# Kernel tuning notes

Hardware: AMD Instinct MI355X
Metric: run time of the kernel (lower is better)

## Reference

```python
import jax, jax.numpy as jnp
import numpy as np

N_NODES = 10000
IN_CH = 512
HID = 128
HEADS = 4
OUT_CH = 256
N_EDGES = 160000
NEG_SLOPE = 0.2  # PyG GATConv default


def gat_conv(x, src, dst, W, a_src, a_dst, b):
    """PyG-style GATConv. x:[N,F_in], W:[F_in,H*C], a_src/a_dst:[H,C], b:[H*C].
    src/dst already include self-loops. Returns [N, H*C] (concat heads)."""
    N = x.shape[0]
    H, C = a_src.shape
    h = (x @ W).reshape(N, H, C)                     # [N,H,C]
    e_src = jnp.einsum('nhc,hc->nh', h, a_src)        # [N,H]
    e_dst = jnp.einsum('nhc,hc->nh', h, a_dst)
    alpha = jax.nn.leaky_relu(e_src[src] + e_dst[dst], NEG_SLOPE)  # [E,H]
    # softmax over incoming edges of each destination node
    m = jax.ops.segment_max(alpha, dst, num_segments=N)            # [N,H]
    ex = jnp.exp(alpha - m[dst])
    denom = jax.ops.segment_sum(ex, dst, num_segments=N)           # [N,H]
    coeff = ex / (denom[dst] + 1e-16)                              # [E,H]
    out = jax.ops.segment_sum(coeff[:, :, None] * h[src], dst, num_segments=N)  # [N,H,C]
    return out.reshape(N, H * C) + b


def _edges_with_self_loops(edge_index, n):
    loops = jnp.arange(n, dtype=edge_index.dtype)
    src = jnp.concatenate([edge_index[0], loops])
    dst = jnp.concatenate([edge_index[1], loops])
    return src, dst


def setup_inputs() -> dict:
    key = jax.random.key(0)
    ks = jax.random.split(key, 20)
    s = 0.05
    inp = {
        'x': jax.random.normal(ks[0], (N_NODES, IN_CH), jnp.float32),
        'W1': jax.random.normal(ks[1], (IN_CH, HEADS * HID), jnp.float32) * s,
        'a1s': jax.random.normal(ks[2], (HEADS, HID), jnp.float32) * s,
        'a1d': jax.random.normal(ks[3], (HEADS, HID), jnp.float32) * s,
        'b1': jnp.zeros((HEADS * HID,), jnp.float32),
        'W2': jax.random.normal(ks[4], (HEADS * HID, HEADS * HID), jnp.float32) * s,
        'a2s': jax.random.normal(ks[5], (HEADS, HID), jnp.float32) * s,
        'a2d': jax.random.normal(ks[6], (HEADS, HID), jnp.float32) * s,
        'b2': jnp.zeros((HEADS * HID,), jnp.float32),
        'W3': jax.random.normal(ks[7], (HEADS * HID, HID), jnp.float32) * s,
        'a3s': jax.random.normal(ks[8], (1, HID), jnp.float32) * s,
        'a3d': jax.random.normal(ks[9], (1, HID), jnp.float32) * s,
        'b3': jnp.zeros((HID,), jnp.float32),
        'Wl': jax.random.normal(ks[10], (HID, OUT_CH), jnp.float32) * s,
        'bl': jnp.zeros((OUT_CH,), jnp.float32),
        'Wr': jax.random.normal(ks[11], (IN_CH, OUT_CH), jnp.float32) * s,
        'br': jnp.zeros((OUT_CH,), jnp.float32),
        'edge_index': jax.random.randint(ks[12], (2, N_EDGES), 0, N_NODES, jnp.int64 if jax.config.jax_enable_x64 else jnp.int32),
    }
    return inp


def reference(x, W1, a1s, a1d, b1, W2, a2s, a2d, b2, W3, a3s, a3d, b3, Wl, bl, Wr, br, edge_index):
    src, dst = _edges_with_self_loops(edge_index, x.shape[0])
    residual = x @ Wr + br
    h = jax.nn.elu(gat_conv(x, src, dst, W1, a1s, a1d, b1))
    h = jax.nn.elu(gat_conv(h, src, dst, W2, a2s, a2d, b2))
    h = jax.nn.elu(gat_conv(h, src, dst, W3, a3s, a3d, b3))
    return h @ Wl + bl + residual
```

## Files before the change

kernel.cpp:

```cpp
#include <hip/hip_runtime.h>
#include <hip/hip_bf16.h>
#include <cstdint>
#include <cstddef>

#define N_NODES 10000
#define M_PAD   10240
#define HEADS   4

typedef __bf16 bfrag8 __attribute__((ext_vector_type(8)));
typedef __bf16 bfrag2 __attribute__((ext_vector_type(2)));
typedef float  floatx4 __attribute__((ext_vector_type(4)));
typedef float  floatx2 __attribute__((ext_vector_type(2)));

#define S0V (M_PAD * 512 / 8)
#define S1E (512 * 512 / 8)
#define S2E (512 * 512 / 8)
#define S3E (512 * 128 / 8)
#define S4E (128 * 256 / 8)
#define S5E (512 * 256 / 8)


__global__ __launch_bounds__(256) void prep(const float* __restrict__ x,
                                            const float* __restrict__ W1,
                                            const float* __restrict__ W2,
                                            const float* __restrict__ W3,
                                            const float* __restrict__ Wl,
                                            const float* __restrict__ Wr,
                                            const int* __restrict__ edst, int E,
                                            __bf16* __restrict__ xb,
                                            __bf16* __restrict__ W1T,
                                            __bf16* __restrict__ W2T,
                                            __bf16* __restrict__ W3T,
                                            __bf16* __restrict__ WlT,
                                            __bf16* __restrict__ WrT,
                                            int* __restrict__ deg) {
    int i = blockIdx.x * 256 + threadIdx.x;
    if (i < S0V) {
        int base = i * 8;
        int row = base >> 9;
        bfrag8 r = {};
        if (row < N_NODES) {
            float4 f0 = ((const float4*)x)[i * 2];
            float4 f1 = ((const float4*)x)[i * 2 + 1];
            r[0] = (__bf16)f0.x; r[1] = (__bf16)f0.y; r[2] = (__bf16)f0.z; r[3] = (__bf16)f0.w;
            r[4] = (__bf16)f1.x; r[5] = (__bf16)f1.y; r[6] = (__bf16)f1.z; r[7] = (__bf16)f1.w;
        }
        *(bfrag8*)(xb + base) = r;
    } else if ((i -= S0V) < S1E) {
        int n = i & 511, kb = (i >> 9) * 8;
        bfrag8 r;
#pragma unroll
        for (int t = 0; t < 8; ++t) r[t] = (__bf16)W1[(kb + t) * 512 + n];
        *(bfrag8*)(W1T + n * 512 + kb) = r;
    } else if ((i -= S1E) < S2E) {
        int n = i & 511, kb = (i >> 9) * 8;
        bfrag8 r;
#pragma unroll
        for (int t = 0; t < 8; ++t) r[t] = (__bf16)W2[(kb + t) * 512 + n];
        *(bfrag8*)(W2T + n * 512 + kb) = r;
    } else if ((i -= S2E) < S3E) {
        int n = i & 127, kb = (i >> 7) * 8;
        bfrag8 r;
#pragma unroll
        for (int t = 0; t < 8; ++t) r[t] = (__bf16)W3[(kb + t) * 128 + n];
        *(bfrag8*)(W3T + n * 512 + kb) = r;
    } else if ((i -= S3E) < S4E) {
        int n = i & 255, kb = (i >> 8) * 8;
        bfrag8 r;
#pragma unroll
        for (int t = 0; t < 8; ++t) r[t] = (__bf16)Wl[(kb + t) * 256 + n];
        *(bfrag8*)(WlT + n * 128 + kb) = r;
    } else if ((i -= S4E) < S5E) {
        int n = i & 255, kb = (i >> 8) * 8;
        bfrag8 r;
#pragma unroll
        for (int t = 0; t < 8; ++t) r[t] = (__bf16)Wr[(kb + t) * 256 + n];
        *(bfrag8*)(WrT + n * 512 + kb) = r;
    } else if ((i -= S5E) < E) {
        atomicAdd(&deg[edst[i]], 1);
    }
}


__global__ __launch_bounds__(1024) void scan_kernel(const int* __restrict__ deg,
                                                    int* __restrict__ rowptr,
                                                    int* __restrict__ cursor, int n) {
    __shared__ int wtot[16], woff[16];
    int t = threadIdx.x, lane = t & 63, wv = t >> 6;
    int chunk = (n + 1023) / 1024;
    int beg = t * chunk, end = beg + chunk; if (end > n) end = n; if (beg > n) beg = n;
    int s = 0;
    for (int i = beg; i < end; ++i) s += deg[i] + 1;
    int v = s;
#pragma unroll
    for (int off = 1; off < 64; off <<= 1) {
        int o = __shfl_up(v, off);
        if (lane >= off) v += o;
    }
    if (lane == 63) wtot[wv] = v;
    __syncthreads();
    if (t == 0) {
        int r = 0;
#pragma unroll
        for (int i = 0; i < 16; ++i) { woff[i] = r; r += wtot[i]; }
        rowptr[n] = r;
    }
    __syncthreads();
    int off = woff[wv] + v - s;
    for (int i = beg; i < end; ++i) {
        rowptr[i] = off; cursor[i] = off;
        off += deg[i] + 1;
    }
}


template <int NT>
__device__ __forceinline__ void gemm_loop(const __bf16* __restrict__ A,
                                          const __bf16* __restrict__ BT, int K,
                                          int m0, int n0, int wave, int lane,
                                          __bf16* As, __bf16* Bs,
                                          floatx4 (&acc)[2][NT]) {
    int r = wave * 8 + (lane >> 3);
    int kof = (lane & 7) * 8;
    const __bf16* gA = A + (size_t)(m0 + r) * K + kof;
    const __bf16* gB = BT + (size_t)(n0 + r) * K + kof;
    __bf16* lA = As + r * 64 + kof;
    __bf16* lB = Bs + r * 64 + kof;
    const __bf16* fA = As + (wave * 32 + (lane & 15)) * 64 + (lane >> 4) * 8;
    const __bf16* fB = Bs + (lane & 15) * 64 + (lane >> 4) * 8;

    for (int k0 = 0; k0 < K; k0 += 64) {
#pragma unroll
        for (int u = 0; u < 4; ++u)
            __builtin_amdgcn_global_load_lds(
                (const __attribute__((address_space(1))) void*)(gA + (size_t)u * 32 * K),
                (__attribute__((address_space(3))) void*)(lA + u * 32 * 64), 16, 0, 0);
#pragma unroll
        for (int u = 0; u < NT / 2; ++u)
            __builtin_amdgcn_global_load_lds(
                (const __attribute__((address_space(1))) void*)(gB + (size_t)u * 32 * K),
                (__attribute__((address_space(3))) void*)(lB + u * 32 * 64), 16, 0, 0);
        gA += 64; gB += 64;
        __syncthreads();

#pragma unroll
        for (int ks = 0; ks < 2; ++ks) {
            bfrag8 a0 = *(const bfrag8*)(fA + ks * 32);
            bfrag8 a1 = *(const bfrag8*)(fA + 16 * 64 + ks * 32);
#pragma unroll
            for (int nt = 0; nt < NT; ++nt) {
                bfrag8 b = *(const bfrag8*)(fB + nt * 16 * 64 + ks * 32);
                acc[0][nt] = __builtin_amdgcn_mfma_f32_16x16x32_bf16(a0, b, acc[0][nt], 0, 0, 0);
                acc[1][nt] = __builtin_amdgcn_mfma_f32_16x16x32_bf16(a1, b, acc[1][nt], 0, 0, 0);
            }
        }
        __syncthreads();
    }
}

__device__ __forceinline__ void gemm_h_tile(const __bf16* __restrict__ A,
                                            const __bf16* __restrict__ BT,
                                            unsigned char* __restrict__ C8,
                                            int N, int K, int H,
                                            const float* __restrict__ as_,
                                            const float* __restrict__ ad_,
                                            float* __restrict__ esp,
                                            float* __restrict__ edp,
                                            int t, __bf16* As, __bf16* Bs,
                                            int wave, int lane) {
    int m0 = (t % 80) * 128, n0 = (t / 80) * 128;
    floatx4 acc[2][8] = {};
    gemm_loop<8>(A, BT, K, m0, n0, wave, lane, As, Bs, acc);

    int crow = m0 + wave * 32 + (lane >> 4) * 4;
    int ccol = n0 + (lane & 15);
#pragma unroll
    for (int mt = 0; mt < 2; ++mt)
#pragma unroll
        for (int nt = 0; nt < 8; ++nt)
#pragma unroll
            for (int r = 0; r < 4; ++r) {
                float v = acc[mt][nt][r];
                size_t o = (size_t)(crow + mt * 16 + r) * N + ccol + nt * 16;
                int p = __builtin_amdgcn_cvt_pk_fp8_f32(v, v, 0, false);
                C8[o] = (unsigned char)(p & 0xff);
            }

    int head = n0 >> 7;
    float a_sv[8], a_dv[8];
#pragma unroll
    for (int nt = 0; nt < 8; ++nt) {
        int cin = nt * 16 + (lane & 15);
        a_sv[nt] = as_[head * 128 + cin];
        a_dv[nt] = ad_[head * 128 + cin];
    }
#pragma unroll
    for (int mt = 0; mt < 2; ++mt)
#pragma unroll
        for (int r = 0; r < 4; ++r) {
            float ps = 0.f, pd = 0.f;
#pragma unroll
            for (int nt = 0; nt < 8; ++nt) {
                float v = acc[mt][nt][r];
                ps += v * a_sv[nt];
                pd += v * a_dv[nt];
            }
#pragma unroll
            for (int off = 8; off; off >>= 1) {
                ps += __shfl_xor(ps, off);
                pd += __shfl_xor(pd, off);
            }
            if ((lane & 15) == 0) {
                int row = crow + mt * 16 + r;
                esp[row * H + head] = ps;
                edp[row * H + head] = pd;
            }
        }
}

__global__ __launch_bounds__(256) void gemm_h(const __bf16* __restrict__ A,
                                              const __bf16* __restrict__ BT,
                                              unsigned char* __restrict__ C8,
                                              int N, int K, int H,
                                              const float* __restrict__ as_,
                                              const float* __restrict__ ad_,
                                              float* __restrict__ esp,
                                              float* __restrict__ edp) {
    __shared__ __align__(16) __bf16 As[128 * 64];
    __shared__ __align__(16) __bf16 Bs[128 * 64];
    int tid = threadIdx.x, wave = tid >> 6, lane = tid & 63;
    int t = blockIdx.x + 80 * blockIdx.y;
    gemm_h_tile(A, BT, C8, N, K, H, as_, ad_, esp, edp, t, As, Bs, wave, lane);
}

__global__ __launch_bounds__(256) void gemm1s(const __bf16* __restrict__ A,
                                              const __bf16* __restrict__ BT,
                                              unsigned char* __restrict__ C8,
                                              const float* __restrict__ as_,
                                              const float* __restrict__ ad_,
                                              float* __restrict__ esp,
                                              float* __restrict__ edp,
                                              const int* __restrict__ esrc,
                                              const int* __restrict__ edst, int E,
                                              int* __restrict__ cursor,
                                              int* __restrict__ csr) {
    __shared__ __align__(16) __bf16 As[128 * 64];
    __shared__ __align__(16) __bf16 Bs[128 * 64];
    int bid = blockIdx.x;
    if (bid >= 320) {
        int i = (bid - 320) * 256 + threadIdx.x;
        if (i < E) {
            int pos = atomicAdd(&cursor[edst[i]], 1);
            csr[pos] = esrc[i];
        } else if (i < E + N_NODES) {
            int v = i - E;
            int pos = atomicAdd(&cursor[v], 1);
            csr[pos] = v;
        }
        return;
    }
    int tid = threadIdx.x, wave = tid >> 6, lane = tid & 63;
    gemm_h_tile(A, BT, C8, 512, 512, 4, as_, ad_, esp, edp, bid, As, Bs, wave, lane);
}

__global__ __launch_bounds__(256) void gemm3r(const __bf16* __restrict__ hb,
                                              const __bf16* __restrict__ W3T,
                                              unsigned char* __restrict__ C8,
                                              const float* __restrict__ a3s,
                                              const float* __restrict__ a3d,
                                              float* __restrict__ esp,
                                              float* __restrict__ edp,
                                              const __bf16* __restrict__ xb,
                                              const __bf16* __restrict__ WrT,
                                              const float* __restrict__ br,
                                              float* __restrict__ out) {
    __shared__ __align__(16) __bf16 As[128 * 64];
    __shared__ __align__(16) __bf16 Bs[128 * 64];
    int tid = threadIdx.x, wave = tid >> 6, lane = tid & 63;
    int bid = blockIdx.x;
    if (bid < 80) {
        gemm_h_tile(hb, W3T, C8, 128, 512, 1, a3s, a3d, esp, edp, bid, As, Bs, wave, lane);
        return;
    }
    int t = bid - 80;
    int m0 = (t % 80) * 128, n0 = (t / 80) * 64;
    floatx4 acc[2][4] = {};
    gemm_loop<4>(xb, WrT, 512, m0, n0, wave, lane, As, Bs, acc);

    int crow = m0 + wave * 32 + (lane >> 4) * 4;
    int ccol = n0 + (lane & 15);
#pragma unroll
    for (int mt = 0; mt < 2; ++mt)
#pragma unroll
        for (int nt = 0; nt < 4; ++nt)
#pragma unroll
            for (int r = 0; r < 4; ++r) {
                int row = crow + mt * 16 + r;
                int col = ccol + nt * 16;
                if (row < N_NODES)
                    out[(size_t)row * 256 + col] = acc[mt][nt][r] + br[col];
            }
}

__global__ __launch_bounds__(256) void gemm_acc(const __bf16* __restrict__ hb3,
                                                const __bf16* __restrict__ WlT,
                                                float* __restrict__ out,
                                                const float* __restrict__ bl) {
    __shared__ __align__(16) __bf16 As[128 * 64];
    __shared__ __align__(16) __bf16 Bs[64 * 64];
    int tid = threadIdx.x, wave = tid >> 6, lane = tid & 63;
    int m0 = blockIdx.x * 128, n0 = blockIdx.y * 64;
    floatx4 acc[2][4] = {};
    gemm_loop<4>(hb3, WlT, 128, m0, n0, wave, lane, As, Bs, acc);

    int crow = m0 + wave * 32 + (lane >> 4) * 4;
    int ccol = n0 + (lane & 15);
#pragma unroll
    for (int mt = 0; mt < 2; ++mt)
#pragma unroll
        for (int nt = 0; nt < 4; ++nt)
#pragma unroll
            for (int r = 0; r < 4; ++r) {
                int row = crow + mt * 16 + r;
                int col = ccol + nt * 16;
                if (row < N_NODES) {
                    size_t o = (size_t)row * 256 + col;
                    out[o] = out[o] + acc[mt][nt][r] + bl[col];
                }
            }
}


template <int H>
__global__ __launch_bounds__(256) void gather_agg(const unsigned char* __restrict__ H8,
                                                  const float* __restrict__ esp,
                                                  const float* __restrict__ edp,
                                                  const int* __restrict__ rowptr,
                                                  const int* __restrict__ csr,
                                                  const float* __restrict__ bias,
                                                  __bf16* __restrict__ outb) {
    constexpr int F = H * 128;
    constexpr int CH = F / 64;
    __shared__ int   sIdx[4][64];
    __shared__ float sWgt[4][64 * H];
    int wave = threadIdx.x >> 6, lane = threadIdx.x & 63;
    int node = blockIdx.x * 4 + wave;
    if (node >= M_PAD) return;
    __bf16* op = outb + (size_t)node * F + lane * CH;
    if (node >= N_NODES) {
        if (H == 4) { bfrag8 z = {}; *(bfrag8*)op = z; }
        else        { bfrag2 z = {}; *(bfrag2*)op = z; }
        return;
    }
    int hsel = (H == 4) ? (lane >> 4) : 0;
    const unsigned char* hp = H8 + lane * CH;
    int beg = rowptr[node], end = rowptr[node + 1];
    float acc[CH] = {};
    float wsum = 0.f;

    float edv0 = 0.f, edv1 = 0.f, edv2 = 0.f, edv3 = 0.f;
    if (H == 4) {
        float4 e4 = *(const float4*)(edp + node * 4);
        edv0 = e4.x; edv1 = e4.y; edv2 = e4.z; edv3 = e4.w;
    } else {
        edv0 = edp[node];
    }

    for (int t0 = beg; t0 < end; t0 += 64) {
        int n_t = end - t0; if (n_t > 64) n_t = 64;
        if (lane < n_t) {
            int s = csr[t0 + lane];
            sIdx[wave][lane] = s;
            if (H == 4) {
                float4 es = *(const float4*)(esp + s * 4);
                float tt0 = es.x + edv0; tt0 = tt0 > 0.f ? tt0 : 0.2f * tt0;
                float tt1 = es.y + edv1; tt1 = tt1 > 0.f ? tt1 : 0.2f * tt1;
                float tt2 = es.z + edv2; tt2 = tt2 > 0.f ? tt2 : 0.2f * tt2;
                float tt3 = es.w + edv3; tt3 = tt3 > 0.f ? tt3 : 0.2f * tt3;
                floatx4 w4 = { __expf(tt0), __expf(tt1), __expf(tt2), __expf(tt3) };
                *(floatx4*)&sWgt[wave][lane * 4] = w4;
            } else {
                float tt = esp[s] + edv0; tt = tt > 0.f ? tt : 0.2f * tt;
                sWgt[wave][lane] = __expf(tt);
            }
        }
        asm volatile("s_waitcnt lgkmcnt(0)" ::: "memory");

        int e = 0;
        for (; e + 3 < n_t; e += 4) {
            int s4[4]; float w4[4];
#pragma unroll
            for (int u = 0; u < 4; ++u) {
                s4[u] = sIdx[wave][e + u];
                w4[u] = sWgt[wave][(e + u) * H + hsel];
            }
            if (H == 4) {
                uint2 p4[4];
#pragma unroll
                for (int u = 0; u < 4; ++u) p4[u] = *(const uint2*)(hp + (size_t)s4[u] * F);
#pragma unroll
                for (int u = 0; u < 4; ++u) {
                    float wgt = w4[u];
                    wsum += wgt;
                    floatx2 f0 = __builtin_amdgcn_cvt_pk_f32_fp8(p4[u].x, false);
                    floatx2 f1 = __builtin_amdgcn_cvt_pk_f32_fp8(p4[u].x, true);
                    floatx2 f2 = __builtin_amdgcn_cvt_pk_f32_fp8(p4[u].y, false);
                    floatx2 f3 = __builtin_amdgcn_cvt_pk_f32_fp8(p4[u].y, true);
                    acc[0] += wgt * f0[0]; acc[1] += wgt * f0[1];
                    acc[2] += wgt * f1[0]; acc[3] += wgt * f1[1];
                    acc[4] += wgt * f2[0]; acc[5] += wgt * f2[1];
                    acc[6] += wgt * f3[0]; acc[7] += wgt * f3[1];
                }
            } else {
                unsigned short p4[4];
#pragma unroll
                for (int u = 0; u < 4; ++u) p4[u] = *(const unsigned short*)(hp + (size_t)s4[u] * F);
#pragma unroll
                for (int u = 0; u < 4; ++u) {
                    float wgt = w4[u];
                    wsum += wgt;
                    floatx2 f0 = __builtin_amdgcn_cvt_pk_f32_fp8((int)p4[u], false);
                    acc[0] += wgt * f0[0]; acc[1] += wgt * f0[1];
                }
            }
        }
        for (; e < n_t; ++e) {
            int s0 = sIdx[wave][e];
            float wgt = sWgt[wave][e * H + hsel];
            wsum += wgt;
            if (H == 4) {
                uint2 p = *(const uint2*)(hp + (size_t)s0 * F);
                floatx2 f0 = __builtin_amdgcn_cvt_pk_f32_fp8(p.x, false);
                floatx2 f1 = __builtin_amdgcn_cvt_pk_f32_fp8(p.x, true);
                floatx2 f2 = __builtin_amdgcn_cvt_pk_f32_fp8(p.y, false);
                floatx2 f3 = __builtin_amdgcn_cvt_pk_f32_fp8(p.y, true);
                acc[0] += wgt * f0[0]; acc[1] += wgt * f0[1];
                acc[2] += wgt * f1[0]; acc[3] += wgt * f1[1];
                acc[4] += wgt * f2[0]; acc[5] += wgt * f2[1];
                acc[6] += wgt * f3[0]; acc[7] += wgt * f3[1];
            } else {
                unsigned short p = *(const unsigned short*)(hp + (size_t)s0 * F);
                floatx2 f0 = __builtin_amdgcn_cvt_pk_f32_fp8((int)p, false);
                acc[0] += wgt * f0[0]; acc[1] += wgt * f0[1];
            }
        }
    }

    float inv = 1.f / (wsum + 1e-16f);
    if (H == 4) {
        bfrag8 r;
#pragma unroll
        for (int k = 0; k < 8; ++k) {
            float o = acc[k] * inv + bias[lane * 8 + k];
            o = o > 0.f ? o : __expf(o) - 1.f;
            r[k] = (__bf16)o;
        }
        *(bfrag8*)op = r;
    } else {
        bfrag2 r;
#pragma unroll
        for (int k = 0; k < 2; ++k) {
            float o = acc[k] * inv + bias[lane * 2 + k];
            o = o > 0.f ? o : __expf(o) - 1.f;
            r[k] = (__bf16)o;
        }
        *(bfrag2*)op = r;
    }
}


extern "C" void kernel_launch(void* const* d_in, const int* in_sizes, int n_in,
                              void* d_out, int out_size, void* d_ws, size_t ws_size,
                              hipStream_t stream) {
    const float* x   = (const float*)d_in[0];
    const float* W1  = (const float*)d_in[1];
    const float* a1s = (const float*)d_in[2];
    const float* a1d = (const float*)d_in[3];
    const float* b1  = (const float*)d_in[4];
    const float* W2  = (const float*)d_in[5];
    const float* a2s = (const float*)d_in[6];
    const float* a2d = (const float*)d_in[7];
    const float* b2  = (const float*)d_in[8];
    const float* W3  = (const float*)d_in[9];
    const float* a3s = (const float*)d_in[10];
    const float* a3d = (const float*)d_in[11];
    const float* b3  = (const float*)d_in[12];
    const float* Wl  = (const float*)d_in[13];
    const float* bl  = (const float*)d_in[14];
    const float* Wr  = (const float*)d_in[15];
    const float* br  = (const float*)d_in[16];
    const int*   ei  = (const int*)d_in[17];
    const int E = in_sizes[17] / 2;
    const int* esrc = ei;
    const int* edst = ei + E;
    const int slots = E + N_NODES;
    float* out = (float*)d_out;

    char* w = (char*)d_ws;
    auto alloc = [&](size_t b) { char* p = w; w += (b + 255) & ~(size_t)255; return p; };
    __bf16* xb  = (__bf16*)alloc((size_t)M_PAD * 512 * 2);
    __bf16* hb  = (__bf16*)alloc((size_t)M_PAD * 512 * 2);
    __bf16* hb3 = (__bf16*)alloc((size_t)M_PAD * 128 * 2);
    unsigned char* Hi8 = (unsigned char*)alloc((size_t)M_PAD * 512);
    __bf16* W1T = (__bf16*)alloc(512 * 512 * 2);
    __bf16* W2T = (__bf16*)alloc(512 * 512 * 2);
    __bf16* W3T = (__bf16*)alloc(128 * 512 * 2);
    __bf16* WlT = (__bf16*)alloc(256 * 128 * 2);
    __bf16* WrT = (__bf16*)alloc(256 * 512 * 2);
    float* esp    = (float*)alloc((size_t)M_PAD * HEADS * 4);
    float* edp    = (float*)alloc((size_t)M_PAD * HEADS * 4);
    int*   deg    = (int*)alloc(N_NODES * 4);
    int*   rowptr = (int*)alloc((N_NODES + 1) * 4);
    int*   cursor = (int*)alloc(N_NODES * 4);
    int*   csr    = (int*)alloc((size_t)slots * 4);

    (void)hipMemsetAsync(deg, 0, N_NODES * sizeof(int), stream);

    const int sp_total = S0V + S1E + S2E + S3E + S4E + S5E + E;
    prep<<<(sp_total + 255) / 256, 256, 0, stream>>>(x, W1, W2, W3, Wl, Wr, edst, E,
                                                     xb, W1T, W2T, W3T, WlT, WrT, deg);
    scan_kernel<<<1, 1024, 0, stream>>>(deg, rowptr, cursor, N_NODES);

    const int scat_blocks = (E + N_NODES + 255) / 256;
    gemm1s<<<320 + scat_blocks, 256, 0, stream>>>(xb, W1T, Hi8, a1s, a1d, esp, edp,
                                                  esrc, edst, E, cursor, csr);
    gather_agg<4><<<M_PAD / 4, 256, 0, stream>>>(Hi8, esp, edp, rowptr, csr, b1, hb);
    gemm_h<<<dim3(80, 4), 256, 0, stream>>>(hb, W2T, Hi8, 512, 512, 4,
                                            a2s, a2d, esp, edp);
    gather_agg<4><<<M_PAD / 4, 256, 0, stream>>>(Hi8, esp, edp, rowptr, csr, b2, hb);
    gemm3r<<<400, 256, 0, stream>>>(hb, W3T, Hi8, a3s, a3d, esp, edp,
                                    xb, WrT, br, out);
    gather_agg<1><<<M_PAD / 4, 256, 0, stream>>>(Hi8, esp, edp, rowptr, csr, b3, hb3);
    gemm_acc<<<dim3(80, 4), 256, 0, stream>>>(hb3, WlT, out, bl);
}
```

Baseline: 236.0 us.

## Fuse final linear layer into last GAT aggregation kernel

Removes the separate gemm_acc MFMA kernel and the Wl transpose in prep. The last gather_agg now stages each node's 128-wide ELU output in shared memory, and each wave computes that node's 256 outputs with fp32 FMAs against Wl read from global memory, accumulating into the output. This saves a kernel launch and the hb3 round trip, but replaces tensor-core matmul with per-node scalar FMAs that re-read Wl (128 KB) for every node. Synchronization uses only an lgkmcnt wait within a wave.

After: 262.6 us. 11.2% more time.

```diff
diff --git a/kernel.cpp b/kernel.cpp
--- a/kernel.cpp
+++ b/kernel.cpp
@@ -16,7 +16,6 @@
 #define S1E (512 * 512 / 8)
 #define S2E (512 * 512 / 8)
 #define S3E (512 * 128 / 8)
-#define S4E (128 * 256 / 8)
 #define S5E (512 * 256 / 8)
 
 
@@ -24,14 +23,12 @@
                                             const float* __restrict__ W1,
                                             const float* __restrict__ W2,
                                             const float* __restrict__ W3,
-                                            const float* __restrict__ Wl,
                                             const float* __restrict__ Wr,
                                             const int* __restrict__ edst, int E,
                                             __bf16* __restrict__ xb,
                                             __bf16* __restrict__ W1T,
                                             __bf16* __restrict__ W2T,
                                             __bf16* __restrict__ W3T,
-                                            __bf16* __restrict__ WlT,
                                             __bf16* __restrict__ WrT,
                                             int* __restrict__ deg) {
     int i = blockIdx.x * 256 + threadIdx.x;
@@ -64,13 +61,7 @@
 #pragma unroll
         for (int t = 0; t < 8; ++t) r[t] = (__bf16)W3[(kb + t) * 128 + n];
         *(bfrag8*)(W3T + n * 512 + kb) = r;
-    } else if ((i -= S3E) < S4E) {
-        int n = i & 255, kb = (i >> 8) * 8;
-        bfrag8 r;
-#pragma unroll
-        for (int t = 0; t < 8; ++t) r[t] = (__bf16)Wl[(kb + t) * 256 + n];
-        *(bfrag8*)(WlT + n * 128 + kb) = r;
-    } else if ((i -= S4E) < S5E) {
+    } else if ((i -= S3E) < S5E) {
         int n = i & 255, kb = (i >> 8) * 8;
         bfrag8 r;
 #pragma unroll
@@ -302,34 +293,6 @@
             }
 }
 
-__global__ __launch_bounds__(256) void gemm_acc(const __bf16* __restrict__ hb3,
-                                                const __bf16* __restrict__ WlT,
-                                                float* __restrict__ out,
-                                                const float* __restrict__ bl) {
-    __shared__ __align__(16) __bf16 As[128 * 64];
-    __shared__ __align__(16) __bf16 Bs[64 * 64];
-    int tid = threadIdx.x, wave = tid >> 6, lane = tid & 63;
-    int m0 = blockIdx.x * 128, n0 = blockIdx.y * 64;
-    floatx4 acc[2][4] = {};
-    gemm_loop<4>(hb3, WlT, 128, m0, n0, wave, lane, As, Bs, acc);
-
-    int crow = m0 + wave * 32 + (lane >> 4) * 4;
-    int ccol = n0 + (lane & 15);
-#pragma unroll
-    for (int mt = 0; mt < 2; ++mt)
-#pragma unroll
-        for (int nt = 0; nt < 4; ++nt)
-#pragma unroll
-            for (int r = 0; r < 4; ++r) {
-                int row = crow + mt * 16 + r;
-                int col = ccol + nt * 16;
-                if (row < N_NODES) {
-                    size_t o = (size_t)row * 256 + col;
-                    out[o] = out[o] + acc[mt][nt][r] + bl[col];
-                }
-            }
-}
-
 
 template <int H>
 __global__ __launch_bounds__(256) void gather_agg(const unsigned char* __restrict__ H8,
@@ -338,18 +301,23 @@
                                                   const int* __restrict__ rowptr,
                                                   const int* __restrict__ csr,
                                                   const float* __restrict__ bias,
-                                                  __bf16* __restrict__ outb) {
+                                                  __bf16* __restrict__ outb,
+                                                  const float* __restrict__ Wl,
+                                                  const float* __restrict__ bl,
+                                                  float* __restrict__ outf) {
     constexpr int F = H * 128;
     constexpr int CH = F / 64;
     __shared__ int   sIdx[4][64];
     __shared__ float sWgt[4][64 * H];
+    __shared__ float sH3[4][128];
     int wave = threadIdx.x >> 6, lane = threadIdx.x & 63;
     int node = blockIdx.x * 4 + wave;
     if (node >= M_PAD) return;
-    __bf16* op = outb + (size_t)node * F + lane * CH;
     if (node >= N_NODES) {
-        if (H == 4) { bfrag8 z = {}; *(bfrag8*)op = z; }
-        else        { bfrag2 z = {}; *(bfrag2*)op = z; }
+        if (H == 4) {
+            bfrag8 z = {};
+            *(bfrag8*)(outb + (size_t)node * F + lane * CH) = z;
+        }
         return;
     }
     int hsel = (H == 4) ? (lane >> 4) : 0;
@@ -455,16 +423,28 @@
             o = o > 0.f ? o : __expf(o) - 1.f;
             r[k] = (__bf16)o;
         }
-        *(bfrag8*)op = r;
+        *(bfrag8*)(outb + (size_t)node * F + lane * CH) = r;
     } else {
-        bfrag2 r;
-#pragma unroll
-        for (int k = 0; k < 2; ++k) {
-            float o = acc[k] * inv + bias[lane * 2 + k];
-            o = o > 0.f ? o : __expf(o) - 1.f;
-            r[k] = (__bf16)o;
-        }
-        *(bfrag2*)op = r;
+        float o0 = acc[0] * inv + bias[lane * 2];
+        float o1 = acc[1] * inv + bias[lane * 2 + 1];
+        o0 = o0 > 0.f ? o0 : __expf(o0) - 1.f;
+        o1 = o1 > 0.f ? o1 : __expf(o1) - 1.f;
+        sH3[wave][lane * 2]     = o0;
+        sH3[wave][lane * 2 + 1] = o1;
+        asm volatile("s_waitcnt lgkmcnt(0)" ::: "memory");
+
+        float4 a = *(const float4*)(bl + lane * 4);
+        const float* wp = Wl + lane * 4;
+#pragma unroll 4
+        for (int k = 0; k < 128; ++k) {
+            float h = sH3[wave][k];
+            float4 wl = *(const float4*)(wp + k * 256);
+            a.x += h * wl.x; a.y += h * wl.y; a.z += h * wl.z; a.w += h * wl.w;
+        }
+        float4* op = (float4*)(outf + (size_t)node * 256 + lane * 4);
+        float4 cur = *op;
+        cur.x += a.x; cur.y += a.y; cur.z += a.z; cur.w += a.w;
+        *op = cur;
     }
 }
 
@@ -500,12 +480,10 @@
     auto alloc = [&](size_t b) { char* p = w; w += (b + 255) & ~(size_t)255; return p; };
     __bf16* xb  = (__bf16*)alloc((size_t)M_PAD * 512 * 2);
     __bf16* hb  = (__bf16*)alloc((size_t)M_PAD * 512 * 2);
-    __bf16* hb3 = (__bf16*)alloc((size_t)M_PAD * 128 * 2);
     unsigned char* Hi8 = (unsigned char*)alloc((size_t)M_PAD * 512);
     __bf16* W1T = (__bf16*)alloc(512 * 512 * 2);
     __bf16* W2T = (__bf16*)alloc(512 * 512 * 2);
     __bf16* W3T = (__bf16*)alloc(128 * 512 * 2);
-    __bf16* WlT = (__bf16*)alloc(256 * 128 * 2);
     __bf16* WrT = (__bf16*)alloc(256 * 512 * 2);
     float* esp    = (float*)alloc((size_t)M_PAD * HEADS * 4);
     float* edp    = (float*)alloc((size_t)M_PAD * HEADS * 4);
@@ -516,20 +494,22 @@
 
     (void)hipMemsetAsync(deg, 0, N_NODES * sizeof(int), stream);
 
-    const int sp_total = S0V + S1E + S2E + S3E + S4E + S5E + E;
-    prep<<<(sp_total + 255) / 256, 256, 0, stream>>>(x, W1, W2, W3, Wl, Wr, edst, E,
-                                                     xb, W1T, W2T, W3T, WlT, WrT, deg);
+    const int sp_total = S0V + S1E + S2E + S3E + S5E + E;
+    prep<<<(sp_total + 255) / 256, 256, 0, stream>>>(x, W1, W2, W3, Wr, edst, E,
+                                                     xb, W1T, W2T, W3T, WrT, deg);
     scan_kernel<<<1, 1024, 0, stream>>>(deg, rowptr, cursor, N_NODES);
 
     const int scat_blocks = (E + N_NODES + 255) / 256;
     gemm1s<<<320 + scat_blocks, 256, 0, stream>>>(xb, W1T, Hi8, a1s, a1d, esp, edp,
                                                   esrc, edst, E, cursor, csr);
-    gather_agg<4><<<M_PAD / 4, 256, 0, stream>>>(Hi8, esp, edp, rowptr, csr, b1, hb);
+    gather_agg<4><<<M_PAD / 4, 256, 0, stream>>>(Hi8, esp, edp, rowptr, csr, b1, hb,
+                                                 nullptr, nullptr, nullptr);
     gemm_h<<<dim3(80, 4), 256, 0, stream>>>(hb, W2T, Hi8, 512, 512, 4,
                                             a2s, a2d, esp, edp);
-    gather_agg<4><<<M_PAD / 4, 256, 0, stream>>>(Hi8, esp, edp, rowptr, csr, b2, hb);
+    gather_agg<4><<<M_PAD / 4, 256, 0, stream>>>(Hi8, esp, edp, rowptr, csr, b2, hb,
+                                                 nullptr, nullptr, nullptr);
     gemm3r<<<400, 256, 0, stream>>>(hb, W3T, Hi8, a3s, a3d, esp, edp,
                                     xb, WrT, br, out);
-    gather_agg<1><<<M_PAD / 4, 256, 0, stream>>>(Hi8, esp, edp, rowptr, csr, b3, hb3);
-    gemm_acc<<<dim3(80, 4), 256, 0, stream>>>(hb3, WlT, out, bl);
-}
+    gather_agg<1><<<M_PAD / 4, 256, 0, stream>>>(Hi8, esp, edp, rowptr, csr, b3,
+                                                 nullptr, Wl, bl, out);
+}
```
